# Optimization experiments

Hardware: AMD Instinct MI355X
Metric: run time of the kernel (lower is better)

## Reference

```python
import jax, jax.numpy as jnp
import numpy as np
from jax.scipy.special import logsumexp

D_MODEL = 512
NHEAD = 8
BATCH = 2
SEQ = 1024


def _safe_log_relu(v):
    # log(max(v, 0)) with well-defined (zero) gradient where v <= 0
    pos = v > 0
    return jnp.where(pos, jnp.log(jnp.where(pos, v, 1.0)), -jnp.inf)


def _split_heads(t, h):
    b, l, hd = t.shape
    return t.reshape(b, l, h, hd // h).transpose(0, 2, 1, 3)  # (B,H,L,d)


def setup_inputs() -> dict:
    key = jax.random.key(0)
    ks = jax.random.split(key, 9)
    s = 1.0 / np.sqrt(D_MODEL)
    x = jax.random.normal(ks[0], (BATCH, SEQ, D_MODEL), jnp.float32)
    mk = lambda k: jax.random.normal(k, (D_MODEL, D_MODEL), jnp.float32) * s
    mb = lambda k: jax.random.normal(k, (D_MODEL,), jnp.float32) * 0.02
    return {
        "x": x,
        "W_Q": mk(ks[1]), "b_Q": mb(ks[2]),
        "W_K": mk(ks[3]), "b_K": mb(ks[4]),
        "W_V": mk(ks[5]), "b_V": mb(ks[6]),
        "W_O": mk(ks[7]), "b_O": mb(ks[8]),
    }


def reference(x, W_Q, b_Q, W_K, b_K, W_V, b_V, W_O, b_O):
    # self-attention: queries = keys = values = x
    Q = _split_heads(x @ W_Q.T + b_Q, NHEAD)  # (B,H,L,D)
    K = _split_heads(x @ W_K.T + b_K, NHEAD)  # (B,H,L,D)
    V = _split_heads(x @ W_V.T + b_V, NHEAD)  # (B,H,L,Dv)

    # normalizer: log sum_j sum_d exp(Q_id) * exp(K_jd)
    log_B = logsumexp(Q + logsumexp(K, axis=-2, keepdims=True), axis=-1)  # (B,H,L)

    log_V_plus = _safe_log_relu(V)[..., None, :]    # (B,H,L,1,Dv)
    log_V_minus = _safe_log_relu(-V)[..., None, :]  # (B,H,L,1,Dv)

    # reduce over key positions: (B,H,L,D,Dv) -> (B,H,D,Dv)
    lse_KV_plus = logsumexp(K[..., :, :, None] + log_V_plus, axis=-3)
    lse_KV_minus = logsumexp(K[..., :, :, None] + log_V_minus, axis=-3)

    # reduce over feature dim D: (B,H,L,D,Dv) -> (B,H,L,Dv)
    log_A_plus = logsumexp(Q[..., None] + lse_KV_plus[..., None, :, :], axis=-2)
    log_A_minus = logsumexp(Q[..., None] + lse_KV_minus[..., None, :, :], axis=-2)

    heads = jnp.exp(log_A_plus - log_B[..., None]) - jnp.exp(log_A_minus - log_B[..., None])

    b, h, l, dv = heads.shape
    joined = heads.transpose(0, 2, 1, 3).reshape(b, l, h * dv)
    return joined @ W_O.T + b_O
```

## Files before the change

kernel.cpp:

```cpp
#include <hip/hip_runtime.h>
#include <math.h>

#define DM   512
#define NH   8
#define HD   64
#define B_   2
#define L_   1024
#define M_   (B_ * L_)

typedef __attribute__((ext_vector_type(8))) short  bfrag;
typedef __attribute__((ext_vector_type(4))) float  fv4;
typedef __attribute__((ext_vector_type(4))) unsigned short usv4;

__device__ __forceinline__ unsigned short f32_bf16_rne(float f) {
    unsigned u = __float_as_uint(f);
    unsigned r = u + 0x7FFF + ((u >> 16) & 1);
    return (unsigned short)(r >> 16);
}
__device__ __forceinline__ float bf16_f32(unsigned short h) {
    return __uint_as_float(((unsigned)h) << 16);
}

#define TM 128
#define TN 64
#define TK 32
#define LDA 40

__device__ __forceinline__ void mfma_gemm(const float* __restrict__ A,
                                          const float* __restrict__ W,
                                          const float* __restrict__ bias,
                                          float* __restrict__ C) {
    __shared__ __align__(16) unsigned short Ah[TM * LDA];
    __shared__ __align__(16) unsigned short Al[TM * LDA];
    __shared__ __align__(16) unsigned short Bh[TN * LDA];
    __shared__ __align__(16) unsigned short Bl[TN * LDA];

    const int tid  = threadIdx.x;
    const int wave = tid >> 6, lane = tid & 63;
    const int quad = lane >> 4, r16 = lane & 15;
    const int m0 = blockIdx.y * TM, n0 = blockIdx.x * TN;

    fv4 acc[2][4] = {};

    for (int k0 = 0; k0 < DM; k0 += TK) {
#pragma unroll
        for (int t = 0; t < 4; ++t) {
            int idx = tid + t * 256;
            int row = idx >> 3, kc = (idx & 7) << 2;
            float4 v = *(const float4*)(A + (size_t)(m0 + row) * DM + k0 + kc);
            usv4 h, l;
            h.x = f32_bf16_rne(v.x); l.x = f32_bf16_rne(v.x - bf16_f32(h.x));
            h.y = f32_bf16_rne(v.y); l.y = f32_bf16_rne(v.y - bf16_f32(h.y));
            h.z = f32_bf16_rne(v.z); l.z = f32_bf16_rne(v.z - bf16_f32(h.z));
            h.w = f32_bf16_rne(v.w); l.w = f32_bf16_rne(v.w - bf16_f32(h.w));
            *(usv4*)(Ah + row * LDA + kc) = h;
            *(usv4*)(Al + row * LDA + kc) = l;
        }
#pragma unroll
        for (int t = 0; t < 2; ++t) {
            int idx = tid + t * 256;
            int row = idx >> 3, kc = (idx & 7) << 2;
            float4 v = *(const float4*)(W + (size_t)(n0 + row) * DM + k0 + kc);
            usv4 h, l;
            h.x = f32_bf16_rne(v.x); l.x = f32_bf16_rne(v.x - bf16_f32(h.x));
            h.y = f32_bf16_rne(v.y); l.y = f32_bf16_rne(v.y - bf16_f32(h.y));
            h.z = f32_bf16_rne(v.z); l.z = f32_bf16_rne(v.z - bf16_f32(h.z));
            h.w = f32_bf16_rne(v.w); l.w = f32_bf16_rne(v.w - bf16_f32(h.w));
            *(usv4*)(Bh + row * LDA + kc) = h;
            *(usv4*)(Bl + row * LDA + kc) = l;
        }
        __syncthreads();

        bfrag ah[2], al[2], bh[4], bl[4];
#pragma unroll
        for (int i = 0; i < 2; ++i) {
            int off = (wave * 32 + i * 16 + r16) * LDA + quad * 8;
            ah[i] = *(const bfrag*)(Ah + off);
            al[i] = *(const bfrag*)(Al + off);
        }
#pragma unroll
        for (int j = 0; j < 4; ++j) {
            int off = (j * 16 + r16) * LDA + quad * 8;
            bh[j] = *(const bfrag*)(Bh + off);
            bl[j] = *(const bfrag*)(Bl + off);
        }

#pragma unroll
        for (int i = 0; i < 2; ++i)
#pragma unroll
            for (int j = 0; j < 4; ++j) {
                acc[i][j] = __builtin_amdgcn_mfma_f32_16x16x32_bf16(ah[i], bh[j], acc[i][j], 0, 0, 0);
                acc[i][j] = __builtin_amdgcn_mfma_f32_16x16x32_bf16(ah[i], bl[j], acc[i][j], 0, 0, 0);
                acc[i][j] = __builtin_amdgcn_mfma_f32_16x16x32_bf16(al[i], bh[j], acc[i][j], 0, 0, 0);
            }
        __syncthreads();
    }

#pragma unroll
    for (int j = 0; j < 4; ++j) {
        int n = n0 + j * 16 + r16;
        float bn = bias[n];
#pragma unroll
        for (int i = 0; i < 2; ++i) {
#pragma unroll
            for (int r = 0; r < 4; ++r) {
                int m = m0 + wave * 32 + i * 16 + quad * 4 + r;
                C[(size_t)m * DM + n] = acc[i][j][r] + bn;
            }
        }
    }
}

__global__ __launch_bounds__(256) void gemm_qkv_kernel(
    const float* __restrict__ x,
    const float* __restrict__ Wq, const float* __restrict__ bq,
    const float* __restrict__ Wk, const float* __restrict__ bk,
    const float* __restrict__ Wv, const float* __restrict__ bv,
    float* __restrict__ Q, float* __restrict__ K, float* __restrict__ V) {
    const float* W; const float* b; float* C;
    if (blockIdx.z == 0)      { W = Wq; b = bq; C = Q; }
    else if (blockIdx.z == 1) { W = Wk; b = bk; C = K; }
    else                      { W = Wv; b = bv; C = V; }
    mfma_gemm(x, W, b, C);
}

__global__ __launch_bounds__(256) void gemm_out_kernel(
    const float* __restrict__ A, const float* __restrict__ W,
    const float* __restrict__ bias, float* __restrict__ C) {
    mfma_gemm(A, W, bias, C);
}

#define JT 64
__global__ __launch_bounds__(256) void kv_stats_kernel(
    const float* __restrict__ Kbuf, const float* __restrict__ Vbuf,
    float* __restrict__ Spart, float* __restrict__ zpart) {
    const int split = blockIdx.x, bh = blockIdx.y;
    const int b = bh >> 3, h = bh & 7;
    const int j0 = split * JT;

    __shared__ float EK[JT][HD + 1];
    __shared__ float VS[JT][HD + 1];

    const int tid = threadIdx.x;
#pragma unroll
    for (int t = 0; t < 4; ++t) {
        int idx = tid + t * 256;
        int r = idx >> 4;
        int c = (idx & 15) << 2;
        size_t row = (size_t)(b * L_ + j0 + r) * DM + h * HD + c;
        float4 kv = *(const float4*)(Kbuf + row);
        EK[r][c + 0] = __expf(kv.x); EK[r][c + 1] = __expf(kv.y);
        EK[r][c + 2] = __expf(kv.z); EK[r][c + 3] = __expf(kv.w);
        float4 vv = *(const float4*)(Vbuf + row);
        VS[r][c + 0] = vv.x; VS[r][c + 1] = vv.y;
        VS[r][c + 2] = vv.z; VS[r][c + 3] = vv.w;
    }
    __syncthreads();

    const int tx = tid & 15, ty = tid >> 4;
    float acc[4][4] = {{0.f}};
#pragma unroll 8
    for (int jj = 0; jj < JT; ++jj) {
        float ek[4], vs[4];
#pragma unroll
        for (int i = 0; i < 4; ++i) ek[i] = EK[jj][ty * 4 + i];
#pragma unroll
        for (int j = 0; j < 4; ++j) vs[j] = VS[jj][tx * 4 + j];
#pragma unroll
        for (int i = 0; i < 4; ++i)
#pragma unroll
            for (int j = 0; j < 4; ++j) acc[i][j] += ek[i] * vs[j];
    }

    float* sp = Spart + ((size_t)bh * 16 + split) * (HD * HD);
#pragma unroll
    for (int i = 0; i < 4; ++i) {
        float4 o; o.x = acc[i][0]; o.y = acc[i][1]; o.z = acc[i][2]; o.w = acc[i][3];
        *(float4*)(sp + (ty * 4 + i) * HD + tx * 4) = o;
    }
    if (tid < HD) {
        float z = 0.f;
#pragma unroll 8
        for (int jj = 0; jj < JT; ++jj) z += EK[jj][tid];
        zpart[((size_t)bh * 16 + split) * HD + tid] = z;
    }
}

__global__ __launch_bounds__(256) void heads_kernel(
    const float* __restrict__ Qbuf, const float* __restrict__ Spart,
    const float* __restrict__ zpart, float* __restrict__ joined) {
    const int tileI = blockIdx.x, bh = blockIdx.y;
    const int b = bh >> 3, h = bh & 7;

    __shared__ float S[HD][HD + 1];
    __shared__ float zl[HD];

    const int tid = threadIdx.x;
#pragma unroll
    for (int t = 0; t < 16; ++t) {
        int idx = tid + t * 256;
        float s = 0.f;
        const float* sp = Spart + (size_t)bh * 16 * (HD * HD) + idx;
#pragma unroll
        for (int p = 0; p < 16; ++p) s += sp[(size_t)p * (HD * HD)];
        S[idx >> 6][idx & 63] = s;
    }
    if (tid < HD) {
        float z = 0.f;
        const float* zp = zpart + (size_t)bh * 16 * HD + tid;
#pragma unroll
        for (int p = 0; p < 16; ++p) z += zp[(size_t)p * HD];
        zl[tid] = z;
    }
    __syncthreads();

    const int lane = tid & 63, w = tid >> 6;
#pragma unroll 1
    for (int r = 0; r < 16; ++r) {
        int i = tileI * 64 + w * 16 + r;
        float q = Qbuf[(size_t)(b * L_ + i) * DM + h * HD + lane];
        float eq = __expf(q);

        float denom = eq * zl[lane];
#pragma unroll
        for (int off = 32; off; off >>= 1) denom += __shfl_xor(denom, off, 64);

        float acc = 0.f;
#pragma unroll
        for (int d = 0; d < HD; ++d) {
            float bq = __shfl(eq, d, 64);
            acc += bq * S[d][lane];
        }
        joined[(size_t)(b * L_ + i) * DM + h * HD + lane] = acc / denom;
    }
}

extern "C" void kernel_launch(void* const* d_in, const int* in_sizes, int n_in,
                              void* d_out, int out_size, void* d_ws, size_t ws_size,
                              hipStream_t stream) {
    const float* x  = (const float*)d_in[0];
    const float* Wq = (const float*)d_in[1];
    const float* bq = (const float*)d_in[2];
    const float* Wk = (const float*)d_in[3];
    const float* bk = (const float*)d_in[4];
    const float* Wv = (const float*)d_in[5];
    const float* bv = (const float*)d_in[6];
    const float* Wo = (const float*)d_in[7];
    const float* bo = (const float*)d_in[8];
    float* out = (float*)d_out;

    float* ws = (float*)d_ws;
    const size_t NQ = (size_t)M_ * DM;
    float* Q      = ws;
    float* K      = ws + NQ;
    float* V      = ws + 2 * NQ;
    float* joined = ws + 3 * NQ;
    float* Spart  = ws + 4 * NQ;
    float* zpart  = ws + 5 * NQ;

    dim3 gQKV(DM / TN, M_ / TM, 3);
    gemm_qkv_kernel<<<gQKV, 256, 0, stream>>>(x, Wq, bq, Wk, bk, Wv, bv, Q, K, V);

    kv_stats_kernel<<<dim3(16, 16), 256, 0, stream>>>(K, V, Spart, zpart);

    heads_kernel<<<dim3(16, 16), 256, 0, stream>>>(Q, Spart, zpart, joined);

    dim3 gO(DM / TN, M_ / TM, 1);
    gemm_out_kernel<<<gO, 256, 0, stream>>>(joined, Wo, bo, out);
}
```

Before: 150.6 us.

## Pre-split inputs and weights into bf16 hi/lo and fuse exp into GEMM epilogue

Adds a prep kernel that converts x and all four weight matrices once into bf16 high/low pairs, so the GEMM tile loaders copy bf16 directly instead of converting fp32 per tile. The QKV GEMM epilogue now applies exp to Q and K, which removes exp from the stats and heads kernels. The heads kernel writes its output as bf16 hi/lo for the output GEMM. This removes repeated conversion work inside the GEMMs at the cost of an extra launch and more workspace traffic.

```diff
diff --git a/kernel.cpp b/kernel.cpp
--- a/kernel.cpp
+++ b/kernel.cpp
@@ -11,6 +11,7 @@
 typedef __attribute__((ext_vector_type(8))) short  bfrag;
 typedef __attribute__((ext_vector_type(4))) float  fv4;
 typedef __attribute__((ext_vector_type(4))) unsigned short usv4;
+typedef __attribute__((ext_vector_type(8))) unsigned short usv8;
 
 __device__ __forceinline__ unsigned short f32_bf16_rne(float f) {
     unsigned u = __float_as_uint(f);
@@ -21,15 +22,44 @@
     return __uint_as_float(((unsigned)h) << 16);
 }
 
+__global__ __launch_bounds__(256) void prep_kernel(
+    const float* __restrict__ x,
+    const float* __restrict__ Wq, const float* __restrict__ Wk,
+    const float* __restrict__ Wv, const float* __restrict__ Wo,
+    unsigned short* __restrict__ xh, unsigned short* __restrict__ xl,
+    unsigned short* __restrict__ wh, unsigned short* __restrict__ wl) {
+    int bid = blockIdx.x;
+    const float* src; unsigned short *dh, *dl; size_t off;
+    if (bid < 1024) {
+        src = x; dh = xh; dl = xl; off = (size_t)bid * 1024;
+    } else {
+        int wsel = (bid - 1024) >> 8;
+        int wb   = (bid - 1024) & 255;
+        src = (wsel == 0) ? Wq : (wsel == 1) ? Wk : (wsel == 2) ? Wv : Wo;
+        dh = wh + (size_t)wsel * 262144;
+        dl = wl + (size_t)wsel * 262144;
+        off = (size_t)wb * 1024;
+    }
+    size_t i = off + (size_t)threadIdx.x * 4;
+    float4 v = *(const float4*)(src + i);
+    usv4 h, l;
+    h.x = f32_bf16_rne(v.x); l.x = f32_bf16_rne(v.x - bf16_f32(h.x));
+    h.y = f32_bf16_rne(v.y); l.y = f32_bf16_rne(v.y - bf16_f32(h.y));
+    h.z = f32_bf16_rne(v.z); l.z = f32_bf16_rne(v.z - bf16_f32(h.z));
+    h.w = f32_bf16_rne(v.w); l.w = f32_bf16_rne(v.w - bf16_f32(h.w));
+    *(usv4*)(dh + i) = h;
+    *(usv4*)(dl + i) = l;
+}
+
 #define TM 128
 #define TN 64
 #define TK 32
 #define LDA 40
 
-__device__ __forceinline__ void mfma_gemm(const float* __restrict__ A,
-                                          const float* __restrict__ W,
-                                          const float* __restrict__ bias,
-                                          float* __restrict__ C) {
+__device__ __forceinline__ void mfma_gemm_bf16(
+    const unsigned short* __restrict__ Ahg, const unsigned short* __restrict__ Alg,
+    const unsigned short* __restrict__ Bhg, const unsigned short* __restrict__ Blg,
+    const float* __restrict__ bias, float* __restrict__ C, int do_exp) {
     __shared__ __align__(16) unsigned short Ah[TM * LDA];
     __shared__ __align__(16) unsigned short Al[TM * LDA];
     __shared__ __align__(16) unsigned short Bh[TN * LDA];
@@ -44,30 +74,18 @@
 
     for (int k0 = 0; k0 < DM; k0 += TK) {
 #pragma unroll
-        for (int t = 0; t < 4; ++t) {
-            int idx = tid + t * 256;
-            int row = idx >> 3, kc = (idx & 7) << 2;
-            float4 v = *(const float4*)(A + (size_t)(m0 + row) * DM + k0 + kc);
-            usv4 h, l;
-            h.x = f32_bf16_rne(v.x); l.x = f32_bf16_rne(v.x - bf16_f32(h.x));
-            h.y = f32_bf16_rne(v.y); l.y = f32_bf16_rne(v.y - bf16_f32(h.y));
-            h.z = f32_bf16_rne(v.z); l.z = f32_bf16_rne(v.z - bf16_f32(h.z));
-            h.w = f32_bf16_rne(v.w); l.w = f32_bf16_rne(v.w - bf16_f32(h.w));
-            *(usv4*)(Ah + row * LDA + kc) = h;
-            *(usv4*)(Al + row * LDA + kc) = l;
-        }
-#pragma unroll
         for (int t = 0; t < 2; ++t) {
             int idx = tid + t * 256;
-            int row = idx >> 3, kc = (idx & 7) << 2;
-            float4 v = *(const float4*)(W + (size_t)(n0 + row) * DM + k0 + kc);
-            usv4 h, l;
-            h.x = f32_bf16_rne(v.x); l.x = f32_bf16_rne(v.x - bf16_f32(h.x));
-            h.y = f32_bf16_rne(v.y); l.y = f32_bf16_rne(v.y - bf16_f32(h.y));
-            h.z = f32_bf16_rne(v.z); l.z = f32_bf16_rne(v.z - bf16_f32(h.z));
-            h.w = f32_bf16_rne(v.w); l.w = f32_bf16_rne(v.w - bf16_f32(h.w));
-            *(usv4*)(Bh + row * LDA + kc) = h;
-            *(usv4*)(Bl + row * LDA + kc) = l;
+            int row = idx >> 2, ch = (idx & 3) << 3;
+            size_t g = (size_t)(m0 + row) * DM + k0 + ch;
+            *(usv8*)(Ah + row * LDA + ch) = *(const usv8*)(Ahg + g);
+            *(usv8*)(Al + row * LDA + ch) = *(const usv8*)(Alg + g);
+        }
+        {
+            int row = tid >> 2, ch = (tid & 3) << 3;
+            size_t g = (size_t)(n0 + row) * DM + k0 + ch;
+            *(usv8*)(Bh + row * LDA + ch) = *(const usv8*)(Bhg + g);
+            *(usv8*)(Bl + row * LDA + ch) = *(const usv8*)(Blg + g);
         }
         __syncthreads();
 
@@ -105,29 +123,32 @@
 #pragma unroll
             for (int r = 0; r < 4; ++r) {
                 int m = m0 + wave * 32 + i * 16 + quad * 4 + r;
-                C[(size_t)m * DM + n] = acc[i][j][r] + bn;
+                float v = acc[i][j][r] + bn;
+                if (do_exp) v = __expf(v);
+                C[(size_t)m * DM + n] = v;
             }
         }
     }
 }
 
 __global__ __launch_bounds__(256) void gemm_qkv_kernel(
-    const float* __restrict__ x,
-    const float* __restrict__ Wq, const float* __restrict__ bq,
-    const float* __restrict__ Wk, const float* __restrict__ bk,
-    const float* __restrict__ Wv, const float* __restrict__ bv,
-    float* __restrict__ Q, float* __restrict__ K, float* __restrict__ V) {
-    const float* W; const float* b; float* C;
-    if (blockIdx.z == 0)      { W = Wq; b = bq; C = Q; }
-    else if (blockIdx.z == 1) { W = Wk; b = bk; C = K; }
-    else                      { W = Wv; b = bv; C = V; }
-    mfma_gemm(x, W, b, C);
+    const unsigned short* __restrict__ xh, const unsigned short* __restrict__ xl,
+    const unsigned short* __restrict__ wh, const unsigned short* __restrict__ wl,
+    const float* __restrict__ bq, const float* __restrict__ bk, const float* __restrict__ bv,
+    float* __restrict__ Qe, float* __restrict__ Ke, float* __restrict__ V) {
+    int z = blockIdx.z;
+    const float* b = (z == 0) ? bq : (z == 1) ? bk : bv;
+    float* C = (z == 0) ? Qe : (z == 1) ? Ke : V;
+    mfma_gemm_bf16(xh, xl, wh + (size_t)z * 262144, wl + (size_t)z * 262144,
+                   b, C, z < 2);
 }
 
 __global__ __launch_bounds__(256) void gemm_out_kernel(
-    const float* __restrict__ A, const float* __restrict__ W,
-    const float* __restrict__ bias, float* __restrict__ C) {
-    mfma_gemm(A, W, bias, C);
+    const unsigned short* __restrict__ jh, const unsigned short* __restrict__ jl,
+    const unsigned short* __restrict__ wh, const unsigned short* __restrict__ wl,
+    const float* __restrict__ bo, float* __restrict__ C) {
+    mfma_gemm_bf16(jh, jl, wh + (size_t)3 * 262144, wl + (size_t)3 * 262144,
+                   bo, C, 0);
 }
 
 #define JT 64
@@ -149,8 +170,8 @@
         int c = (idx & 15) << 2;
         size_t row = (size_t)(b * L_ + j0 + r) * DM + h * HD + c;
         float4 kv = *(const float4*)(Kbuf + row);
-        EK[r][c + 0] = __expf(kv.x); EK[r][c + 1] = __expf(kv.y);
-        EK[r][c + 2] = __expf(kv.z); EK[r][c + 3] = __expf(kv.w);
+        EK[r][c + 0] = kv.x; EK[r][c + 1] = kv.y;
+        EK[r][c + 2] = kv.z; EK[r][c + 3] = kv.w;
         float4 vv = *(const float4*)(Vbuf + row);
         VS[r][c + 0] = vv.x; VS[r][c + 1] = vv.y;
         VS[r][c + 2] = vv.z; VS[r][c + 3] = vv.w;
@@ -188,7 +209,8 @@
 
 __global__ __launch_bounds__(256) void heads_kernel(
     const float* __restrict__ Qbuf, const float* __restrict__ Spart,
-    const float* __restrict__ zpart, float* __restrict__ joined) {
+    const float* __restrict__ zpart,
+    unsigned short* __restrict__ jh, unsigned short* __restrict__ jl) {
     const int tileI = blockIdx.x, bh = blockIdx.y;
     const int b = bh >> 3, h = bh & 7;
 
@@ -218,8 +240,7 @@
 #pragma unroll 1
     for (int r = 0; r < 16; ++r) {
         int i = tileI * 64 + w * 16 + r;
-        float q = Qbuf[(size_t)(b * L_ + i) * DM + h * HD + lane];
-        float eq = __expf(q);
+        float eq = Qbuf[(size_t)(b * L_ + i) * DM + h * HD + lane];
 
         float denom = eq * zl[lane];
 #pragma unroll
@@ -231,7 +252,12 @@
             float bq = __shfl(eq, d, 64);
             acc += bq * S[d][lane];
         }
-        joined[(size_t)(b * L_ + i) * DM + h * HD + lane] = acc / denom;
+        float val = acc / denom;
+        size_t oidx = (size_t)(b * L_ + i) * DM + h * HD + lane;
+        unsigned short hh = f32_bf16_rne(val);
+        unsigned short ll = f32_bf16_rne(val - bf16_f32(hh));
+        jh[oidx] = hh;
+        jl[oidx] = ll;
     }
 }
 
@@ -249,22 +275,30 @@
     const float* bo = (const float*)d_in[8];
     float* out = (float*)d_out;
 
-    float* ws = (float*)d_ws;
+    float* f = (float*)d_ws;
     const size_t NQ = (size_t)M_ * DM;
-    float* Q      = ws;
-    float* K      = ws + NQ;
-    float* V      = ws + 2 * NQ;
-    float* joined = ws + 3 * NQ;
-    float* Spart  = ws + 4 * NQ;
-    float* zpart  = ws + 5 * NQ;
+    float* Qe    = f;
+    float* Ke    = f + NQ;
+    float* V     = f + 2 * NQ;
+    float* Spart = f + 3 * NQ;
+    float* zpart = f + 4 * NQ;
+    unsigned short* u = (unsigned short*)(f + 4 * NQ + 16384);
+    unsigned short* xh = u;
+    unsigned short* xl = u + NQ;
+    unsigned short* wh = u + 2 * NQ;
+    unsigned short* wl = u + 3 * NQ;
+    unsigned short* jh = u + 4 * NQ;
+    unsigned short* jl = u + 5 * NQ;
+
+    prep_kernel<<<2048, 256, 0, stream>>>(x, Wq, Wk, Wv, Wo, xh, xl, wh, wl);
 
     dim3 gQKV(DM / TN, M_ / TM, 3);
-    gemm_qkv_kernel<<<gQKV, 256, 0, stream>>>(x, Wq, bq, Wk, bk, Wv, bv, Q, K, V);
-
-    kv_stats_kernel<<<dim3(16, 16), 256, 0, stream>>>(K, V, Spart, zpart);
-
-    heads_kernel<<<dim3(16, 16), 256, 0, stream>>>(Q, Spart, zpart, joined);
+    gemm_qkv_kernel<<<gQKV, 256, 0, stream>>>(xh, xl, wh, wl, bq, bk, bv, Qe, Ke, V);
+
+    kv_stats_kernel<<<dim3(16, 16), 256, 0, stream>>>(Ke, V, Spart, zpart);
+
+    heads_kernel<<<dim3(16, 16), 256, 0, stream>>>(Qe, Spart, zpart, jh, jl);
 
     dim3 gO(DM / TN, M_ / TM, 1);
-    gemm_out_kernel<<<gO, 256, 0, stream>>>(joined, Wo, bo, out);
-}
+    gemm_out_kernel<<<gO, 256, 0, stream>>>(jh, jl, wh, wl, bo, out);
+}
```

New measurement: 142.5 us. 1.06x faster.
